# Kernel tuning notes

Hardware: AMD Instinct MI355X
Metric: run time of the kernel (lower is better)

Reference implementation:

```python
import jax, jax.numpy as jnp
import numpy as np

B = 262144   # number of (group, item) prediction pairs
M = 16       # max members per group (ragged -> padded)
NU = 100000  # num_users
NI = 50000   # num_items
D = 32       # embedding_dim (hardcoded via torch.zeros([32]))


def setup_inputs() -> dict:
    key = jax.random.key(0)
    ks = jax.random.split(key, 9)
    item_inputs = jax.random.randint(ks[0], (B,), 0, NI)
    member_ids = jax.random.randint(ks[1], (B, M), 0, NU)
    lengths = jax.random.randint(ks[2], (B, 1), 1, M + 1)
    member_mask = jnp.arange(M)[None, :] < lengths  # [B, M] bool, variable group sizes
    user_table = jax.random.normal(ks[3], (NU, D), jnp.float32) * 0.1  # xavier-ish
    item_table = jax.random.normal(ks[4], (NI, D), jnp.float32) * 0.1
    W_bil = jax.random.normal(ks[5], (D, D), jnp.float32)  # nn.Bilinear(D, D, 1) weight[0]
    b_bil = jax.random.normal(ks[6], (1,), jnp.float32) * 0.05
    W1 = jax.random.normal(ks[7], (8, 3 * D), jnp.float32) * 0.05  # Linear(96, 8)
    b1 = jnp.zeros((8,), jnp.float32)
    W2 = jax.random.normal(ks[8], (1, 8), jnp.float32) * 0.05  # Linear(8, 1)
    b2 = jnp.zeros((1,), jnp.float32)
    return {
        "item_inputs": item_inputs, "member_ids": member_ids, "member_mask": member_mask,
        "user_table": user_table, "item_table": item_table,
        "W_bil": W_bil, "b_bil": b_bil, "W1": W1, "b1": b1, "W2": W2, "b2": b2,
    }


def reference(item_inputs, member_ids, member_mask, user_table, item_table,
              W_bil, b_bil, W1, b1, W2, b2):
    item_e = item_table[item_inputs]          # [B, D] gather
    mem_e = user_table[member_ids]            # [B, M, D] gather
    # bilinear attention score per member: m^T W i + b (softmax in original is computed then discarded)
    scores = jnp.einsum('bmd,de,be->bm', mem_e, W_bil, item_e) + b_bil[0]
    w = scores * member_mask.astype(scores.dtype)  # zero out padded members (ragged groups)
    final_user = jnp.einsum('bm,bmd->bd', w, mem_e)  # unnormalized weighted sum of members
    new_embeds = jnp.concatenate([final_user * item_e, final_user, item_e], axis=-1)  # [B, 3D]
    h = jax.nn.relu(new_embeds @ W1.T + b1)
    y = jax.nn.sigmoid(h @ W2.T + b2)          # [B, 1]
    return y
```

## Files before the change

kernel.cpp:

```cpp
#include <hip/hip_runtime.h>
#include <math.h>

#define DD 32
#define MM 16
#define TROW 80

typedef int          vi4 __attribute__((ext_vector_type(4)));
typedef unsigned int vu4 __attribute__((ext_vector_type(4)));

__device__ __forceinline__ void load8f4(const float* __restrict__ p, float* r) {
    const float4* q = (const float4*)p;
#pragma unroll
    for (int i = 0; i < 8; ++i) {
        float4 v = q[i];
        r[4*i+0] = v.x; r[4*i+1] = v.y; r[4*i+2] = v.z; r[4*i+3] = v.w;
    }
}

__global__ void precompute_item(const float* __restrict__ item_table,
                                const float* __restrict__ W_bil,
                                const float* __restrict__ W1,
                                float* __restrict__ tbl, int NI) {
    int g = blockIdx.x * blockDim.x + threadIdx.x;
    if (g >= NI * DD) return;
    int i = g >> 5;
    int d = g & (DD - 1);
    const float* row = item_table + (size_t)i * DD;
    float it[DD];
    load8f4(row, it);
    const float* w = W_bil + d * DD;
    float s0 = 0.f, s1 = 0.f, s2 = 0.f, s3 = 0.f;
#pragma unroll
    for (int e = 0; e < DD; e += 4) {
        s0 = fmaf(w[e+0], it[e+0], s0);
        s1 = fmaf(w[e+1], it[e+1], s1);
        s2 = fmaf(w[e+2], it[e+2], s2);
        s3 = fmaf(w[e+3], it[e+3], s3);
    }
    float* o = tbl + (size_t)i * TROW;
    o[d]      = (s0 + s1) + (s2 + s3);
    o[DD + d] = row[d];
    if (d < 8) {
        const float* w1 = W1 + d * 96 + 64;
        float c0 = 0.f, c1 = 0.f, c2 = 0.f, c3 = 0.f;
#pragma unroll
        for (int e = 0; e < DD; e += 4) {
            c0 = fmaf(w1[e+0], it[e+0], c0);
            c1 = fmaf(w1[e+1], it[e+1], c1);
            c2 = fmaf(w1[e+2], it[e+2], c2);
            c3 = fmaf(w1[e+3], it[e+3], c3);
        }
        o[64 + d] = (c0 + c1) + (c2 + c3);
    }
}

__device__ __forceinline__ void member1(const float* __restrict__ ut, int id,
                                        const float* __restrict__ t, float bb,
                                        float* __restrict__ fin) {
    float me[DD];
    load8f4(ut + (size_t)id * DD, me);
    float s0 = 0.f, s1 = 0.f, s2 = 0.f, s3 = 0.f;
#pragma unroll
    for (int d = 0; d < DD; d += 4) {
        s0 = fmaf(me[d+0], t[d+0], s0);
        s1 = fmaf(me[d+1], t[d+1], s1);
        s2 = fmaf(me[d+2], t[d+2], s2);
        s3 = fmaf(me[d+3], t[d+3], s3);
    }
    float s = ((s0 + s1) + (s2 + s3)) + bb;
#pragma unroll
    for (int d = 0; d < DD; ++d) fin[d] = fmaf(s, me[d], fin[d]);
}

__device__ __forceinline__ void member2(const float* __restrict__ ut, int ia, int ib,
                                        const float* __restrict__ t, float bb,
                                        float* __restrict__ fin) {
    float ma[DD], mb[DD];
    load8f4(ut + (size_t)ia * DD, ma);
    load8f4(ut + (size_t)ib * DD, mb);
    float a0 = 0.f, a1 = 0.f, a2 = 0.f, a3 = 0.f;
    float c0 = 0.f, c1 = 0.f, c2 = 0.f, c3 = 0.f;
#pragma unroll
    for (int d = 0; d < DD; d += 4) {
        a0 = fmaf(ma[d+0], t[d+0], a0);
        a1 = fmaf(ma[d+1], t[d+1], a1);
        a2 = fmaf(ma[d+2], t[d+2], a2);
        a3 = fmaf(ma[d+3], t[d+3], a3);
        c0 = fmaf(mb[d+0], t[d+0], c0);
        c1 = fmaf(mb[d+1], t[d+1], c1);
        c2 = fmaf(mb[d+2], t[d+2], c2);
        c3 = fmaf(mb[d+3], t[d+3], c3);
    }
    float sa = ((a0 + a1) + (a2 + a3)) + bb;
    float sb = ((c0 + c1) + (c2 + c3)) + bb;
#pragma unroll
    for (int d = 0; d < DD; ++d) fin[d] = fmaf(sa, ma[d], fin[d]);
#pragma unroll
    for (int d = 0; d < DD; ++d) fin[d] = fmaf(sb, mb[d], fin[d]);
}

template <bool USE_TBL>
__global__ __launch_bounds__(256)
void bilinear_main(const int* __restrict__ item_inputs,
                   const int* __restrict__ member_ids,
                   const unsigned char* __restrict__ member_mask,
                   const float* __restrict__ user_table,
                   const float* __restrict__ item_table,
                   const float* __restrict__ tbl,
                   const float* __restrict__ W_bil,
                   const float* __restrict__ b_bil,
                   const float* __restrict__ W1,
                   const float* __restrict__ b1v,
                   const float* __restrict__ W2,
                   const float* __restrict__ b2v,
                   float* __restrict__ out, int Btot) {
    int b = blockIdx.x * blockDim.x + threadIdx.x;
    if (b >= Btot) return;

    int item = __builtin_nontemporal_load(item_inputs + b);

    vu4 mv = __builtin_nontemporal_load((const vu4*)(member_mask + (size_t)b * MM));
    int len = __popc(mv[0] & 0x01010101u) + __popc(mv[1] & 0x01010101u) +
              __popc(mv[2] & 0x01010101u) + __popc(mv[3] & 0x01010101u);

    const vi4* mp = (const vi4*)(member_ids + (size_t)b * MM);
    vi4 q0 = __builtin_nontemporal_load(mp + 0);
    vi4 q1 = __builtin_nontemporal_load(mp + 1);
    vi4 q2 = __builtin_nontemporal_load(mp + 2);
    vi4 q3 = __builtin_nontemporal_load(mp + 3);
    int ids[MM];
    ids[0]=q0[0];  ids[1]=q0[1];  ids[2]=q0[2];  ids[3]=q0[3];
    ids[4]=q1[0];  ids[5]=q1[1];  ids[6]=q1[2];  ids[7]=q1[3];
    ids[8]=q2[0];  ids[9]=q2[1];  ids[10]=q2[2]; ids[11]=q2[3];
    ids[12]=q3[0]; ids[13]=q3[1]; ids[14]=q3[2]; ids[15]=q3[3];

    float t[DD];
    const float* tb = nullptr;
    if (USE_TBL) {
        tb = tbl + (size_t)item * TROW;
        load8f4(tb, t);
    } else {
        float it0[DD];
        load8f4(item_table + (size_t)item * DD, it0);
#pragma unroll 4
        for (int d = 0; d < DD; ++d) {
            float s = 0.f;
#pragma unroll
            for (int e = 0; e < DD; ++e) s = fmaf(W_bil[d * DD + e], it0[e], s);
            t[d] = s;
        }
    }

    float bb = b_bil[0];
    float fin[DD];
#pragma unroll
    for (int d = 0; d < DD; ++d) fin[d] = 0.f;

#pragma unroll
    for (int p = 0; p < MM / 2; ++p) {
        int m = 2 * p;
        if (m + 1 < len)      member2(user_table, ids[m], ids[m + 1], t, bb, fin);
        else if (m < len)     member1(user_table, ids[m], t, bb, fin);
    }

    float it[DD];
    float cj[8];
    if (USE_TBL) {
        load8f4(tb + DD, it);
        float4 g0 = *(const float4*)(tb + 64);
        float4 g1 = *(const float4*)(tb + 68);
        cj[0] = g0.x; cj[1] = g0.y; cj[2] = g0.z; cj[3] = g0.w;
        cj[4] = g1.x; cj[5] = g1.y; cj[6] = g1.z; cj[7] = g1.w;
    } else {
        load8f4(item_table + (size_t)item * DD, it);
#pragma unroll
        for (int j = 0; j < 8; ++j) {
            float s = 0.f;
#pragma unroll
            for (int d = 0; d < DD; ++d) s = fmaf(W1[j * 96 + 64 + d], it[d], s);
            cj[j] = s;
        }
    }

    float h[8];
#pragma unroll
    for (int j = 0; j < 8; ++j) h[j] = cj[j] + b1v[j];
#pragma unroll
    for (int d = 0; d < DD; ++d) {
        float f = fin[d];
        float pfi = f * it[d];
#pragma unroll
        for (int j = 0; j < 8; ++j) {
            h[j] = fmaf(W1[j * 96 + d], pfi, h[j]);
            h[j] = fmaf(W1[j * 96 + 32 + d], f, h[j]);
        }
    }
    float z = b2v[0];
#pragma unroll
    for (int j = 0; j < 8; ++j) {
        float hv = h[j] > 0.f ? h[j] : 0.f;
        z = fmaf(W2[j], hv, z);
    }
    __builtin_nontemporal_store(1.f / (1.f + __expf(-z)), out + b);
}

extern "C" void kernel_launch(void* const* d_in, const int* in_sizes, int n_in,
                              void* d_out, int out_size, void* d_ws, size_t ws_size,
                              hipStream_t stream) {
    const int*           item_inputs = (const int*)d_in[0];
    const int*           member_ids  = (const int*)d_in[1];
    const unsigned char* member_mask = (const unsigned char*)d_in[2];
    const float*         user_table  = (const float*)d_in[3];
    const float*         item_table  = (const float*)d_in[4];
    const float*         W_bil       = (const float*)d_in[5];
    const float*         b_bil       = (const float*)d_in[6];
    const float*         W1          = (const float*)d_in[7];
    const float*         b1          = (const float*)d_in[8];
    const float*         W2          = (const float*)d_in[9];
    const float*         b2          = (const float*)d_in[10];
    float* out = (float*)d_out;

    int Btot = in_sizes[0];
    int NI   = in_sizes[4] / DD;

    bool use_tbl = ws_size >= (size_t)NI * TROW * sizeof(float);
    int blk = 256;
    if (use_tbl) {
        float* tbl = (float*)d_ws;
        precompute_item<<<(NI * DD + blk - 1) / blk, blk, 0, stream>>>(item_table, W_bil, W1, tbl, NI);
        bilinear_main<true><<<(Btot + blk - 1) / blk, blk, 0, stream>>>(
            item_inputs, member_ids, member_mask, user_table, item_table, tbl,
            W_bil, b_bil, W1, b1, W2, b2, out, Btot);
    } else {
        bilinear_main<false><<<(Btot + blk - 1) / blk, blk, 0, stream>>>(
            item_inputs, member_ids, member_mask, user_table, item_table, nullptr,
            W_bil, b_bil, W1, b1, W2, b2, out, Btot);
    }
}
```

Before: 170.9 us.

## Split each prediction across four lanes with shuffle reductions

```diff
diff --git a/kernel.cpp b/kernel.cpp
--- a/kernel.cpp
+++ b/kernel.cpp
@@ -6,7 +6,6 @@
 #define TROW 80
 
 typedef int          vi4 __attribute__((ext_vector_type(4)));
-typedef unsigned int vu4 __attribute__((ext_vector_type(4)));
 
 __device__ __forceinline__ void load8f4(const float* __restrict__ p, float* r) {
     const float4* q = (const float4*)p;
@@ -52,51 +51,6 @@
         }
         o[64 + d] = (c0 + c1) + (c2 + c3);
     }
-}
-
-__device__ __forceinline__ void member1(const float* __restrict__ ut, int id,
-                                        const float* __restrict__ t, float bb,
-                                        float* __restrict__ fin) {
-    float me[DD];
-    load8f4(ut + (size_t)id * DD, me);
-    float s0 = 0.f, s1 = 0.f, s2 = 0.f, s3 = 0.f;
-#pragma unroll
-    for (int d = 0; d < DD; d += 4) {
-        s0 = fmaf(me[d+0], t[d+0], s0);
-        s1 = fmaf(me[d+1], t[d+1], s1);
-        s2 = fmaf(me[d+2], t[d+2], s2);
-        s3 = fmaf(me[d+3], t[d+3], s3);
-    }
-    float s = ((s0 + s1) + (s2 + s3)) + bb;
-#pragma unroll
-    for (int d = 0; d < DD; ++d) fin[d] = fmaf(s, me[d], fin[d]);
-}
-
-__device__ __forceinline__ void member2(const float* __restrict__ ut, int ia, int ib,
-                                        const float* __restrict__ t, float bb,
-                                        float* __restrict__ fin) {
-    float ma[DD], mb[DD];
-    load8f4(ut + (size_t)ia * DD, ma);
-    load8f4(ut + (size_t)ib * DD, mb);
-    float a0 = 0.f, a1 = 0.f, a2 = 0.f, a3 = 0.f;
-    float c0 = 0.f, c1 = 0.f, c2 = 0.f, c3 = 0.f;
-#pragma unroll
-    for (int d = 0; d < DD; d += 4) {
-        a0 = fmaf(ma[d+0], t[d+0], a0);
-        a1 = fmaf(ma[d+1], t[d+1], a1);
-        a2 = fmaf(ma[d+2], t[d+2], a2);
-        a3 = fmaf(ma[d+3], t[d+3], a3);
-        c0 = fmaf(mb[d+0], t[d+0], c0);
-        c1 = fmaf(mb[d+1], t[d+1], c1);
-        c2 = fmaf(mb[d+2], t[d+2], c2);
-        c3 = fmaf(mb[d+3], t[d+3], c3);
-    }
-    float sa = ((a0 + a1) + (a2 + a3)) + bb;
-    float sb = ((c0 + c1) + (c2 + c3)) + bb;
-#pragma unroll
-    for (int d = 0; d < DD; ++d) fin[d] = fmaf(sa, ma[d], fin[d]);
-#pragma unroll
-    for (int d = 0; d < DD; ++d) fin[d] = fmaf(sb, mb[d], fin[d]);
 }
 
 template <bool USE_TBL>
@@ -114,25 +68,16 @@
                    const float* __restrict__ W2,
                    const float* __restrict__ b2v,
                    float* __restrict__ out, int Btot) {
-    int b = blockIdx.x * blockDim.x + threadIdx.x;
+    int tid = blockIdx.x * blockDim.x + threadIdx.x;
+    int b = tid >> 2;
+    int q = tid & 3;
     if (b >= Btot) return;
 
     int item = __builtin_nontemporal_load(item_inputs + b);
-
-    vu4 mv = __builtin_nontemporal_load((const vu4*)(member_mask + (size_t)b * MM));
-    int len = __popc(mv[0] & 0x01010101u) + __popc(mv[1] & 0x01010101u) +
-              __popc(mv[2] & 0x01010101u) + __popc(mv[3] & 0x01010101u);
-
-    const vi4* mp = (const vi4*)(member_ids + (size_t)b * MM);
-    vi4 q0 = __builtin_nontemporal_load(mp + 0);
-    vi4 q1 = __builtin_nontemporal_load(mp + 1);
-    vi4 q2 = __builtin_nontemporal_load(mp + 2);
-    vi4 q3 = __builtin_nontemporal_load(mp + 3);
-    int ids[MM];
-    ids[0]=q0[0];  ids[1]=q0[1];  ids[2]=q0[2];  ids[3]=q0[3];
-    ids[4]=q1[0];  ids[5]=q1[1];  ids[6]=q1[2];  ids[7]=q1[3];
-    ids[8]=q2[0];  ids[9]=q2[1];  ids[10]=q2[2]; ids[11]=q2[3];
-    ids[12]=q3[0]; ids[13]=q3[1]; ids[14]=q3[2]; ids[15]=q3[3];
+    unsigned mw = __builtin_nontemporal_load((const unsigned*)member_mask + tid);
+    int cnt = __popc(mw & 0x01010101u);
+    vi4 idv = __builtin_nontemporal_load((const vi4*)member_ids + tid);
+    int id0 = idv[0];
 
     float t[DD];
     const float* tb = nullptr;
@@ -157,51 +102,78 @@
     for (int d = 0; d < DD; ++d) fin[d] = 0.f;
 
 #pragma unroll
-    for (int p = 0; p < MM / 2; ++p) {
-        int m = 2 * p;
-        if (m + 1 < len)      member2(user_table, ids[m], ids[m + 1], t, bb, fin);
-        else if (m < len)     member1(user_table, ids[m], t, bb, fin);
-    }
+    for (int k = 0; k < 4; ++k) {
+        bool act = (k < cnt);
+        int idk = act ? idv[k] : id0;
+        float me[DD];
+        load8f4(user_table + (size_t)idk * DD, me);
+        float s0 = 0.f, s1 = 0.f, s2 = 0.f, s3 = 0.f;
+#pragma unroll
+        for (int d = 0; d < DD; d += 4) {
+            s0 = fmaf(me[d+0], t[d+0], s0);
+            s1 = fmaf(me[d+1], t[d+1], s1);
+            s2 = fmaf(me[d+2], t[d+2], s2);
+            s3 = fmaf(me[d+3], t[d+3], s3);
+        }
+        float s = act ? (((s0 + s1) + (s2 + s3)) + bb) : 0.f;
+#pragma unroll
+        for (int d = 0; d < DD; ++d) fin[d] = fmaf(s, me[d], fin[d]);
+    }
+
+#pragma unroll
+    for (int d = 0; d < DD; ++d) fin[d] += __shfl_xor(fin[d], 1);
+#pragma unroll
+    for (int d = 0; d < DD; ++d) fin[d] += __shfl_xor(fin[d], 2);
 
     float it[DD];
-    float cj[8];
+    load8f4(USE_TBL ? (tb + DD) : (item_table + (size_t)item * DD), it);
+
+    int j0 = 2 * q;
+    float c0, c1;
     if (USE_TBL) {
-        load8f4(tb + DD, it);
-        float4 g0 = *(const float4*)(tb + 64);
-        float4 g1 = *(const float4*)(tb + 68);
-        cj[0] = g0.x; cj[1] = g0.y; cj[2] = g0.z; cj[3] = g0.w;
-        cj[4] = g1.x; cj[5] = g1.y; cj[6] = g1.z; cj[7] = g1.w;
+        c0 = tb[64 + j0];
+        c1 = tb[64 + j0 + 1];
     } else {
-        load8f4(item_table + (size_t)item * DD, it);
-#pragma unroll
-        for (int j = 0; j < 8; ++j) {
-            float s = 0.f;
-#pragma unroll
-            for (int d = 0; d < DD; ++d) s = fmaf(W1[j * 96 + 64 + d], it[d], s);
-            cj[j] = s;
-        }
-    }
-
-    float h[8];
-#pragma unroll
-    for (int j = 0; j < 8; ++j) h[j] = cj[j] + b1v[j];
-#pragma unroll
-    for (int d = 0; d < DD; ++d) {
-        float f = fin[d];
-        float pfi = f * it[d];
-#pragma unroll
-        for (int j = 0; j < 8; ++j) {
-            h[j] = fmaf(W1[j * 96 + d], pfi, h[j]);
-            h[j] = fmaf(W1[j * 96 + 32 + d], f, h[j]);
-        }
-    }
-    float z = b2v[0];
-#pragma unroll
-    for (int j = 0; j < 8; ++j) {
-        float hv = h[j] > 0.f ? h[j] : 0.f;
-        z = fmaf(W2[j], hv, z);
-    }
-    __builtin_nontemporal_store(1.f / (1.f + __expf(-z)), out + b);
+        float a0 = 0.f, a1 = 0.f;
+#pragma unroll
+        for (int d = 0; d < DD; ++d) {
+            a0 = fmaf(W1[j0 * 96 + 64 + d], it[d], a0);
+            a1 = fmaf(W1[(j0 + 1) * 96 + 64 + d], it[d], a1);
+        }
+        c0 = a0; c1 = a1;
+    }
+    float h0 = c0 + b1v[j0];
+    float h1 = c1 + b1v[j0 + 1];
+
+    const float4* w1r0a = (const float4*)(W1 + j0 * 96);
+    const float4* w1r0b = (const float4*)(W1 + j0 * 96 + 32);
+    const float4* w1r1a = (const float4*)(W1 + (j0 + 1) * 96);
+    const float4* w1r1b = (const float4*)(W1 + (j0 + 1) * 96 + 32);
+#pragma unroll
+    for (int dq = 0; dq < 8; ++dq) {
+        float4 wa0 = w1r0a[dq], wb0 = w1r0b[dq];
+        float4 wa1 = w1r1a[dq], wb1 = w1r1b[dq];
+        float f0 = fin[4*dq+0], f1 = fin[4*dq+1], f2 = fin[4*dq+2], f3 = fin[4*dq+3];
+        float p0 = f0 * it[4*dq+0], p1 = f1 * it[4*dq+1];
+        float p2 = f2 * it[4*dq+2], p3 = f3 * it[4*dq+3];
+        h0 = fmaf(wa0.x, p0, h0); h0 = fmaf(wb0.x, f0, h0);
+        h0 = fmaf(wa0.y, p1, h0); h0 = fmaf(wb0.y, f1, h0);
+        h0 = fmaf(wa0.z, p2, h0); h0 = fmaf(wb0.z, f2, h0);
+        h0 = fmaf(wa0.w, p3, h0); h0 = fmaf(wb0.w, f3, h0);
+        h1 = fmaf(wa1.x, p0, h1); h1 = fmaf(wb1.x, f0, h1);
+        h1 = fmaf(wa1.y, p1, h1); h1 = fmaf(wb1.y, f1, h1);
+        h1 = fmaf(wa1.z, p2, h1); h1 = fmaf(wb1.z, f2, h1);
+        h1 = fmaf(wa1.w, p3, h1); h1 = fmaf(wb1.w, f3, h1);
+    }
+    float hv0 = h0 > 0.f ? h0 : 0.f;
+    float hv1 = h1 > 0.f ? h1 : 0.f;
+    float zp = W2[j0] * hv0 + W2[j0 + 1] * hv1;
+    zp += __shfl_xor(zp, 1);
+    zp += __shfl_xor(zp, 2);
+    if (q == 0) {
+        float z = zp + b2v[0];
+        __builtin_nontemporal_store(1.f / (1.f + __expf(-z)), out + b);
+    }
 }
 
 extern "C" void kernel_launch(void* const* d_in, const int* in_sizes, int n_in,
@@ -225,14 +197,15 @@
 
     bool use_tbl = ws_size >= (size_t)NI * TROW * sizeof(float);
     int blk = 256;
+    int nthreads = Btot * 4;
     if (use_tbl) {
         float* tbl = (float*)d_ws;
         precompute_item<<<(NI * DD + blk - 1) / blk, blk, 0, stream>>>(item_table, W_bil, W1, tbl, NI);
-        bilinear_main<true><<<(Btot + blk - 1) / blk, blk, 0, stream>>>(
+        bilinear_main<true><<<(nthreads + blk - 1) / blk, blk, 0, stream>>>(
             item_inputs, member_ids, member_mask, user_table, item_table, tbl,
             W_bil, b_bil, W1, b1, W2, b2, out, Btot);
     } else {
-        bilinear_main<false><<<(Btot + blk - 1) / blk, blk, 0, stream>>>(
+        bilinear_main<false><<<(nthreads + blk - 1) / blk, blk, 0, stream>>>(
             item_inputs, member_ids, member_mask, user_table, item_table, nullptr,
             W_bil, b_bil, W1, b1, W2, b2, out, Btot);
     }
```

Result: slower. 291.3 us (+70.5%).
